# Performance work log

Measured on AMD Instinct MI355X. Metric: run time of the kernel, lower is better.

The kernel has to match this reference:

```python
import jax, jax.numpy as jnp
import numpy as np

M = 19
DIM = 768
D = DIM // 2  # r=2 -> 384
EPS = 1e-5


def _bn_eval(h, gamma, beta):
    # eval-mode BatchNorm1d with running_mean=0, running_var=1
    return h * (gamma / jnp.sqrt(1.0 + EPS)) + beta


def setup_inputs() -> dict:
    key = jax.random.key(0)
    ks = jax.random.split(key, 24)
    s = 0.02
    inp = {
        "x": jax.random.normal(ks[0], (4096, M * DIM), jnp.float32),
        "g": jax.random.normal(ks[1], (4096, M * DIM), jnp.float32),
        # fc: Linear(768,384) -> ReLU -> BN(384) -> Linear(384,384)
        "fc1_W": jax.random.normal(ks[2], (D, DIM), jnp.float32) * s,
        "fc1_b": jnp.zeros((D,), jnp.float32),
        "bn1_g": jnp.ones((D,), jnp.float32),
        "bn1_b": jnp.zeros((D,), jnp.float32),
        "fc2_W": jax.random.normal(ks[3], (D, D), jnp.float32) * s,
        "fc2_b": jnp.zeros((D,), jnp.float32),
        # 19 branch Linears fcs: (d,d); g_fcs: (dim+d, dim)
        "fcs_W": jax.random.normal(ks[4], (M, D, D), jnp.float32) * s,
        "fcs_b": jnp.zeros((M, D), jnp.float32),
        "gfcs_W": jax.random.normal(ks[5], (M, DIM, DIM + D), jnp.float32) * s,
        "gfcs_b": jnp.zeros((M, DIM), jnp.float32),
        # classifier head (numpy_class=20 < 30): 768->128->32->20
        "l1_W": jax.random.normal(ks[6], (128, DIM), jnp.float32) * s,
        "l1_b": jnp.zeros((128,), jnp.float32),
        "bna_g": jnp.ones((128,), jnp.float32),
        "bna_b": jnp.zeros((128,), jnp.float32),
        "l2_W": jax.random.normal(ks[7], (32, 128), jnp.float32) * s,
        "l2_b": jnp.zeros((32,), jnp.float32),
        "bnb_g": jnp.ones((32,), jnp.float32),
        "bnb_b": jnp.zeros((32,), jnp.float32),
        "l3_W": jax.random.normal(ks[8], (20, 32), jnp.float32) * s,
        "l3_b": jnp.zeros((20,), jnp.float32),
    }
    return inp


def reference(x, g, fc1_W, fc1_b, bn1_g, bn1_b, fc2_W, fc2_b,
              fcs_W, fcs_b, gfcs_W, gfcs_b,
              l1_W, l1_b, bna_g, bna_b, l2_W, l2_b, bnb_g, bnb_b, l3_W, l3_b):
    bs = x.shape[0]
    x3 = x.reshape(bs, M, DIM)
    g3 = g.reshape(bs, M, DIM)

    # selective_ts_with_g
    fea_u = jnp.sum(x3, axis=1)                              # (bs, 768)
    h = jax.nn.relu(fea_u @ fc1_W.T + fc1_b)
    h = _bn_eval(h, bn1_g, bn1_b)
    fea_z = h @ fc2_W.T + fc2_b                              # (bs, 384)

    # 19 branch small GEMMs, batched
    vec = jnp.einsum('bd,mod->bmo', fea_z, fcs_W) + fcs_b    # (bs, 19, 384)
    cat = jnp.concatenate([vec, g3], axis=-1)                # (bs, 19, 1152)
    att = jnp.einsum('bmi,moi->bmo', cat, gfcs_W) + gfcs_b   # (bs, 19, 768)
    att = jax.nn.softmax(att, axis=1)                        # softmax over 19 branches
    fea_v = jnp.sum(x3 * att, axis=1)                        # (bs, 768)

    # classifier head
    h = jax.nn.relu(fea_v @ l1_W.T + l1_b)
    h = _bn_eval(h, bna_g, bna_b)
    h = jax.nn.relu(h @ l2_W.T + l2_b)
    h = _bn_eval(h, bnb_g, bnb_b)
    return h @ l3_W.T + l3_b                                 # (bs, 20)
```

## Files before the change

### kernel.cpp

```cpp
#include <hip/hip_runtime.h>


typedef unsigned short u16;
typedef unsigned int u32;
typedef float f32x4 __attribute__((ext_vector_type(4)));
typedef __bf16 bf16x8 __attribute__((ext_vector_type(8)));

#define GPTR(p) ((const __attribute__((address_space(1))) void*)(p))
#define SPTR(p) ((__attribute__((address_space(3))) void*)(p))

__device__ __forceinline__ u16 f2bf(float f) {
    u32 u = __float_as_uint(f);
    u += 0x7fffu + ((u >> 16) & 1u);
    return (u16)(u >> 16);
}
__device__ __forceinline__ float bf2f(u16 h) {
    return __uint_as_float(((u32)h) << 16);
}

#define BNRS 0.9999950000374997f

#define EPI_BIAS    0
#define EPI_RELU_BN 1

template <int EPI>
__global__ __launch_bounds__(256)
void gemm_bf16_kernel(const u16* __restrict__ A, const u16* __restrict__ B,
                      const float* __restrict__ bias,
                      const float* __restrict__ bnG, const float* __restrict__ bnB,
                      u16* __restrict__ C, int K, int N)
{
    constexpr int BK = 32;
    __shared__ __align__(16) u16 lA[128 * BK];
    __shared__ __align__(16) u16 lB[128 * BK];

    const int tid  = threadIdx.x;
    const int wave = tid >> 6;
    const int lane = tid & 63;
    const int bm   = blockIdx.x * 128;
    const int bn   = blockIdx.y * 128;
    const int wm   = (wave >> 1) * 64;
    const int wn   = (wave & 1) * 64;
    const int rl   = lane & 15;
    const int qk   = (lane >> 4) * 8;

    f32x4 acc[4][4] = {};

    const u16* Ab = A + (size_t)bm * K;
    const u16* Bb = B + (size_t)bn * K;

    for (int k0 = 0; k0 < K; k0 += BK) {
#pragma unroll
        for (int r = 0; r < 2; ++r) {
            const int c   = r * 256 + wave * 64 + lane;
            const int row = c >> 2;
            const int kc  = (c & 3) << 3;
            const u16* sa = Ab + (size_t)row * K + (k0 + kc);
            const u16* sb = Bb + (size_t)row * K + (k0 + kc);
            __builtin_amdgcn_global_load_lds(GPTR(sa), SPTR(&lA[(r * 256 + wave * 64) * 8]), 16, 0, 0);
            __builtin_amdgcn_global_load_lds(GPTR(sb), SPTR(&lB[(r * 256 + wave * 64) * 8]), 16, 0, 0);
        }
        __syncthreads();

        bf16x8 af[4], bfr[4];
#pragma unroll
        for (int i = 0; i < 4; ++i) af[i]  = *(const bf16x8*)&lA[(wm + i * 16 + rl) * BK + qk];
#pragma unroll
        for (int j = 0; j < 4; ++j) bfr[j] = *(const bf16x8*)&lB[(wn + j * 16 + rl) * BK + qk];
#pragma unroll
        for (int i = 0; i < 4; ++i)
#pragma unroll
            for (int j = 0; j < 4; ++j)
                acc[i][j] = __builtin_amdgcn_mfma_f32_16x16x32_bf16(af[i], bfr[j], acc[i][j], 0, 0, 0);
        __syncthreads();
    }

    const int q4 = (lane >> 4) * 4;
#pragma unroll
    for (int j = 0; j < 4; ++j) {
        const int col = bn + wn + j * 16 + rl;
        const float bsv = bias[col];
        float scl = 1.f, sft = 0.f;
        if constexpr (EPI == EPI_RELU_BN) { scl = bnG[col] * BNRS; sft = bnB[col]; }
#pragma unroll
        for (int i = 0; i < 4; ++i) {
            const int row0 = bm + wm + i * 16 + q4;
#pragma unroll
            for (int r = 0; r < 4; ++r) {
                float v = acc[i][j][r] + bsv;
                if constexpr (EPI == EPI_RELU_BN) v = fmaxf(v, 0.f) * scl + sft;
                C[(size_t)(row0 + r) * N + col] = f2bf(v);
            }
        }
    }
}

__global__ __launch_bounds__(256)
void att_gemm_kernel(const u16* __restrict__ vec, const float* __restrict__ g,
                     const u16* __restrict__ W, const float* __restrict__ bias,
                     u16* __restrict__ att)
{
    constexpr int BK = 32, K = 1152;
    __shared__ __align__(16) u16 lA[128 * BK];
    __shared__ __align__(16) u16 lB[128 * BK];

    const int m    = blockIdx.z;
    const int tid  = threadIdx.x;
    const int wave = tid >> 6;
    const int lane = tid & 63;
    const int bm   = blockIdx.x * 128;
    const int bn   = blockIdx.y * 128;
    const int wm   = (wave >> 1) * 64;
    const int wn   = (wave & 1) * 64;
    const int rl   = lane & 15;
    const int qk   = (lane >> 4) * 8;

    f32x4 acc[4][4] = {};

    const u16*  Av = vec + (size_t)bm * 7296 + m * 384;
    const float* Ag = g  + (size_t)bm * 14592 + m * 768;
    const u16*  Bb = W  + (size_t)m * 884736 + (size_t)bn * K;

    for (int k0 = 0; k0 < K; k0 += BK) {
        if (k0 < 384) {
#pragma unroll
            for (int r = 0; r < 2; ++r) {
                const int c   = r * 256 + wave * 64 + lane;
                const int row = c >> 2;
                const int kc  = (c & 3) << 3;
                const u16* sa = Av + (size_t)row * 7296 + (k0 + kc);
                __builtin_amdgcn_global_load_lds(GPTR(sa), SPTR(&lA[(r * 256 + wave * 64) * 8]), 16, 0, 0);
            }
        } else {
#pragma unroll
            for (int r = 0; r < 2; ++r) {
                const int c   = r * 256 + tid;
                const int row = c >> 2;
                const int kc  = (c & 3) << 3;
                const float* sf = Ag + (size_t)row * 14592 + (k0 - 384 + kc);
                const float4 f0 = *(const float4*)sf;
                const float4 f1 = *(const float4*)(sf + 4);
                uint4 pk;
                pk.x = (u32)f2bf(f0.x) | ((u32)f2bf(f0.y) << 16);
                pk.y = (u32)f2bf(f0.z) | ((u32)f2bf(f0.w) << 16);
                pk.z = (u32)f2bf(f1.x) | ((u32)f2bf(f1.y) << 16);
                pk.w = (u32)f2bf(f1.z) | ((u32)f2bf(f1.w) << 16);
                *(uint4*)&lA[c * 8] = pk;
            }
        }
#pragma unroll
        for (int r = 0; r < 2; ++r) {
            const int c   = r * 256 + wave * 64 + lane;
            const int row = c >> 2;
            const int kc  = (c & 3) << 3;
            const u16* sb = Bb + (size_t)row * K + (k0 + kc);
            __builtin_amdgcn_global_load_lds(GPTR(sb), SPTR(&lB[(r * 256 + wave * 64) * 8]), 16, 0, 0);
        }
        __syncthreads();

        bf16x8 af[4], bfr[4];
#pragma unroll
        for (int i = 0; i < 4; ++i) af[i]  = *(const bf16x8*)&lA[(wm + i * 16 + rl) * BK + qk];
#pragma unroll
        for (int j = 0; j < 4; ++j) bfr[j] = *(const bf16x8*)&lB[(wn + j * 16 + rl) * BK + qk];
#pragma unroll
        for (int i = 0; i < 4; ++i)
#pragma unroll
            for (int j = 0; j < 4; ++j)
                acc[i][j] = __builtin_amdgcn_mfma_f32_16x16x32_bf16(af[i], bfr[j], acc[i][j], 0, 0, 0);
        __syncthreads();
    }

    const int q4 = (lane >> 4) * 4;
#pragma unroll
    for (int j = 0; j < 4; ++j) {
        const int col = bn + wn + j * 16 + rl;
        const float bsv = bias[(size_t)m * 768 + col];
#pragma unroll
        for (int i = 0; i < 4; ++i) {
            const int row0 = bm + wm + i * 16 + q4;
#pragma unroll
            for (int r = 0; r < 4; ++r) {
                att[(size_t)(row0 + r) * 14592 + m * 768 + col] = f2bf(acc[i][j][r] + bsv);
            }
        }
    }
}

__global__ __launch_bounds__(256)
void cvt_weights_kernel(const float* __restrict__ s0, const float* __restrict__ s1,
                        const float* __restrict__ s2, const float* __restrict__ s3,
                        const float* __restrict__ s4,
                        u16* __restrict__ d0, u16* __restrict__ d1, u16* __restrict__ d2,
                        u16* __restrict__ d3, u16* __restrict__ d4)
{
    const int i = blockIdx.x * 256 + threadIdx.x;
    const float* s; u16* d; int off;
    if (i < 294912)        { s = s0; d = d0; off = i; }
    else if (i < 442368)   { s = s1; d = d1; off = i - 294912; }
    else if (i < 3244032)  { s = s2; d = d2; off = i - 442368; }
    else if (i < 20054016) { s = s3; d = d3; off = i - 3244032; }
    else                   { s = s4; d = d4; off = i - 20054016; }
    d[off] = f2bf(s[off]);
}

__global__ __launch_bounds__(256)
void feau_kernel(const float* __restrict__ x, u16* __restrict__ feau)
{
    const int b = blockIdx.x;
    const int o = blockIdx.y * 256 + threadIdx.x;
    const float* xp = x + (size_t)b * 14592 + o;
    float s = 0.f;
#pragma unroll
    for (int m = 0; m < 19; ++m) s += xp[m * 768];
    feau[(size_t)b * 768 + o] = f2bf(s);
}

__global__ __launch_bounds__(256)
void softmax_feav_kernel(const u16* __restrict__ att, const float* __restrict__ x,
                         u16* __restrict__ feav)
{
    const int b = blockIdx.x;
    const int o = blockIdx.y * 256 + threadIdx.x;
    const u16* ap   = att + (size_t)b * 14592 + o;
    const float* xp = x   + (size_t)b * 14592 + o;
    float l[19];
    float mx = -1e30f;
#pragma unroll
    for (int m = 0; m < 19; ++m) { l[m] = bf2f(ap[m * 768]); mx = fmaxf(mx, l[m]); }
    float s = 0.f;
#pragma unroll
    for (int m = 0; m < 19; ++m) { const float e = __expf(l[m] - mx); l[m] = e; s += e; }
    const float inv = 1.f / s;
    float a = 0.f;
#pragma unroll
    for (int m = 0; m < 19; ++m) a += xp[m * 768] * l[m];
    feav[(size_t)b * 768 + o] = f2bf(a * inv);
}

__global__ __launch_bounds__(256)
void l2_kernel(const u16* __restrict__ h1, const float* __restrict__ W,
               const float* __restrict__ bias, const float* __restrict__ bg,
               const float* __restrict__ bb, float* __restrict__ h2)
{
    const int idx = blockIdx.x * 256 + threadIdx.x;
    const int b = idx >> 5, n = idx & 31;
    const u16* hp  = h1 + (size_t)b * 128;
    const float* wp = W + n * 128;
    float a = bias[n];
#pragma unroll 8
    for (int k = 0; k < 128; ++k) a += bf2f(hp[k]) * wp[k];
    a = fmaxf(a, 0.f) * (bg[n] * BNRS) + bb[n];
    h2[idx] = a;
}

__global__ __launch_bounds__(256)
void l3_kernel(const float* __restrict__ h2, const float* __restrict__ W,
               const float* __restrict__ bias, float* __restrict__ out)
{
    const int idx = blockIdx.x * 256 + threadIdx.x;
    const int b = idx / 20, n = idx - b * 20;
    const float* hp = h2 + (size_t)b * 32;
    const float* wp = W + n * 32;
    float a = bias[n];
#pragma unroll
    for (int k = 0; k < 32; ++k) a += hp[k] * wp[k];
    out[idx] = a;
}

extern "C" void kernel_launch(void* const* d_in, const int* in_sizes, int n_in,
                              void* d_out, int out_size, void* d_ws, size_t ws_size,
                              hipStream_t stream)
{
    const float* x      = (const float*)d_in[0];
    const float* g      = (const float*)d_in[1];
    const float* fc1_W  = (const float*)d_in[2];
    const float* fc1_b  = (const float*)d_in[3];
    const float* bn1_g  = (const float*)d_in[4];
    const float* bn1_b  = (const float*)d_in[5];
    const float* fc2_W  = (const float*)d_in[6];
    const float* fc2_b  = (const float*)d_in[7];
    const float* fcs_W  = (const float*)d_in[8];
    const float* fcs_b  = (const float*)d_in[9];
    const float* gfcs_W = (const float*)d_in[10];
    const float* gfcs_b = (const float*)d_in[11];
    const float* l1_W   = (const float*)d_in[12];
    const float* l1_b   = (const float*)d_in[13];
    const float* bna_g  = (const float*)d_in[14];
    const float* bna_b  = (const float*)d_in[15];
    const float* l2_W   = (const float*)d_in[16];
    const float* l2_b   = (const float*)d_in[17];
    const float* bnb_g  = (const float*)d_in[18];
    const float* bnb_b  = (const float*)d_in[19];
    const float* l3_W   = (const float*)d_in[20];
    const float* l3_b   = (const float*)d_in[21];
    float* out = (float*)d_out;

    char* w = (char*)d_ws;
    size_t off = 0;
    auto alloc = [&](size_t bytes) { void* p = w + off; off += (bytes + 255) & ~(size_t)255; return p; };
    u16* fc1w  = (u16*)alloc(294912ull * 2);
    u16* fc2w  = (u16*)alloc(147456ull * 2);
    u16* fcsw  = (u16*)alloc(2801664ull * 2);
    u16* gfcsw = (u16*)alloc(16809984ull * 2);
    u16* l1w   = (u16*)alloc(98304ull * 2);
    u16* feau  = (u16*)alloc(3145728ull * 2);
    u16* hbuf  = (u16*)alloc(1572864ull * 2);
    u16* feaz  = (u16*)alloc(1572864ull * 2);
    u16* vecb  = (u16*)alloc(29884416ull * 2);
    u16* attb  = (u16*)alloc(59768832ull * 2);
    u16* feav  = (u16*)alloc(3145728ull * 2);
    u16* h1b   = (u16*)alloc(524288ull * 2);
    float* h2f = (float*)alloc(131072ull * 4);
    (void)ws_size; (void)in_sizes; (void)n_in; (void)out_size;

    cvt_weights_kernel<<<78720, 256, 0, stream>>>(fc1_W, fc2_W, fcs_W, gfcs_W, l1_W,
                                                  fc1w, fc2w, fcsw, gfcsw, l1w);
    feau_kernel<<<dim3(4096, 3), 256, 0, stream>>>(x, feau);
    gemm_bf16_kernel<EPI_RELU_BN><<<dim3(32, 3), 256, 0, stream>>>(feau, fc1w, fc1_b, bn1_g, bn1_b, hbuf, 768, 384);
    gemm_bf16_kernel<EPI_BIAS><<<dim3(32, 3), 256, 0, stream>>>(hbuf, fc2w, fc2_b, nullptr, nullptr, feaz, 384, 384);
    gemm_bf16_kernel<EPI_BIAS><<<dim3(32, 57), 256, 0, stream>>>(feaz, fcsw, fcs_b, nullptr, nullptr, vecb, 384, 7296);
    att_gemm_kernel<<<dim3(32, 6, 19), 256, 0, stream>>>(vecb, g, gfcsw, gfcs_b, attb);
    softmax_feav_kernel<<<dim3(4096, 3), 256, 0, stream>>>(attb, x, feav);
    gemm_bf16_kernel<EPI_RELU_BN><<<dim3(32, 1), 256, 0, stream>>>(feav, l1w, l1_b, bna_g, bna_b, h1b, 768, 128);
    l2_kernel<<<512, 256, 0, stream>>>(h1b, l2_W, l2_b, bnb_g, bnb_b, h2f);
    l3_kernel<<<320, 256, 0, stream>>>(h2f, l3_W, l3_b, out);
}
```

Measured before the change: 968.6 us.

## Fold per-branch fcs weights into gfcs weights and pre-convert g to bf16

Composes each branch's fcs Linear with the first 384 columns of its gfcs weight (W1·Wfcs) once per call, with the fcs bias folded into a combined bias. This removes the vec GEMM and its large intermediate buffer, and the attention GEMM now reads fea_z directly. When workspace allows, g is converted to bf16 in a separate pass so the attention GEMM can use async global-to-LDS loads for all of K. feau and softmax are vectorised to 4 elements per thread. The weight-composition GEMM and the g conversion are extra work done on every call.

```diff
diff --git a/kernel.cpp b/kernel.cpp
--- a/kernel.cpp
+++ b/kernel.cpp
@@ -3,6 +3,7 @@
 
 typedef unsigned short u16;
 typedef unsigned int u32;
+typedef long long i64;
 typedef float f32x4 __attribute__((ext_vector_type(4)));
 typedef __bf16 bf16x8 __attribute__((ext_vector_type(8)));
 
@@ -17,23 +18,29 @@
 __device__ __forceinline__ float bf2f(u16 h) {
     return __uint_as_float(((u32)h) << 16);
 }
+__device__ __forceinline__ u32 pk2(float a, float b) {
+    return (u32)f2bf(a) | ((u32)f2bf(b) << 16);
+}
 
 #define BNRS 0.9999950000374997f
 
-#define EPI_BIAS    0
-#define EPI_RELU_BN 1
+#define EPI_NONE    0
+#define EPI_BIAS    1
+#define EPI_RELU_BN 2
 
 template <int EPI>
 __global__ __launch_bounds__(256)
-void gemm_bf16_kernel(const u16* __restrict__ A, const u16* __restrict__ B,
+void gemm_bf16_kernel(const u16* __restrict__ A, i64 Abat, int lda,
+                      const u16* __restrict__ B, i64 Bbat, int ldb,
                       const float* __restrict__ bias,
                       const float* __restrict__ bnG, const float* __restrict__ bnB,
-                      u16* __restrict__ C, int K, int N)
+                      u16* __restrict__ C, i64 Cbat, int ldc, int K)
 {
     constexpr int BK = 32;
     __shared__ __align__(16) u16 lA[128 * BK];
     __shared__ __align__(16) u16 lB[128 * BK];
 
+    const int z    = blockIdx.z;
     const int tid  = threadIdx.x;
     const int wave = tid >> 6;
     const int lane = tid & 63;
@@ -46,8 +53,8 @@
 
     f32x4 acc[4][4] = {};
 
-    const u16* Ab = A + (size_t)bm * K;
-    const u16* Bb = B + (size_t)bn * K;
+    const u16* Ab = A + (size_t)z * Abat + (size_t)bm * lda;
+    const u16* Bb = B + (size_t)z * Bbat + (size_t)bn * ldb;
 
     for (int k0 = 0; k0 < K; k0 += BK) {
 #pragma unroll
@@ -55,8 +62,8 @@
             const int c   = r * 256 + wave * 64 + lane;
             const int row = c >> 2;
             const int kc  = (c & 3) << 3;
-            const u16* sa = Ab + (size_t)row * K + (k0 + kc);
-            const u16* sb = Bb + (size_t)row * K + (k0 + kc);
+            const u16* sa = Ab + (size_t)row * lda + (k0 + kc);
+            const u16* sb = Bb + (size_t)row * ldb + (k0 + kc);
             __builtin_amdgcn_global_load_lds(GPTR(sa), SPTR(&lA[(r * 256 + wave * 64) * 8]), 16, 0, 0);
             __builtin_amdgcn_global_load_lds(GPTR(sb), SPTR(&lB[(r * 256 + wave * 64) * 8]), 16, 0, 0);
         }
@@ -75,30 +82,32 @@
         __syncthreads();
     }
 
+    u16* Cb = C + (size_t)z * Cbat;
     const int q4 = (lane >> 4) * 4;
 #pragma unroll
     for (int j = 0; j < 4; ++j) {
         const int col = bn + wn + j * 16 + rl;
-        const float bsv = bias[col];
-        float scl = 1.f, sft = 0.f;
+        float bsv = 0.f, scl = 1.f, sft = 0.f;
+        if constexpr (EPI != EPI_NONE) bsv = bias[col];
         if constexpr (EPI == EPI_RELU_BN) { scl = bnG[col] * BNRS; sft = bnB[col]; }
 #pragma unroll
         for (int i = 0; i < 4; ++i) {
             const int row0 = bm + wm + i * 16 + q4;
 #pragma unroll
             for (int r = 0; r < 4; ++r) {
-                float v = acc[i][j][r] + bsv;
+                float v = acc[i][j][r];
+                if constexpr (EPI != EPI_NONE) v += bsv;
                 if constexpr (EPI == EPI_RELU_BN) v = fmaxf(v, 0.f) * scl + sft;
-                C[(size_t)(row0 + r) * N + col] = f2bf(v);
+                Cb[(size_t)(row0 + r) * ldc + col] = f2bf(v);
             }
         }
     }
 }
 
 __global__ __launch_bounds__(256)
-void att_gemm_kernel(const u16* __restrict__ vec, const float* __restrict__ g,
-                     const u16* __restrict__ W, const float* __restrict__ bias,
-                     u16* __restrict__ att)
+void att_gemm_a_kernel(const u16* __restrict__ feaz, const u16* __restrict__ gb,
+                       const u16* __restrict__ W, const float* __restrict__ bc,
+                       u16* __restrict__ att)
 {
     constexpr int BK = 32, K = 1152;
     __shared__ __align__(16) u16 lA[128 * BK];
@@ -117,9 +126,78 @@
 
     f32x4 acc[4][4] = {};
 
-    const u16*  Av = vec + (size_t)bm * 7296 + m * 384;
-    const float* Ag = g  + (size_t)bm * 14592 + m * 768;
-    const u16*  Bb = W  + (size_t)m * 884736 + (size_t)bn * K;
+    const u16* A1 = feaz + (size_t)bm * 384;
+    const u16* A2 = gb + (size_t)bm * 14592 + m * 768;
+    const u16* Bb = W + (size_t)m * 884736 + (size_t)bn * K;
+
+    for (int k0 = 0; k0 < K; k0 += BK) {
+#pragma unroll
+        for (int r = 0; r < 2; ++r) {
+            const int c   = r * 256 + wave * 64 + lane;
+            const int row = c >> 2;
+            const int kc  = (c & 3) << 3;
+            const u16* sa = (k0 < 384)
+                ? A1 + (size_t)row * 384 + (k0 + kc)
+                : A2 + (size_t)row * 14592 + (k0 - 384 + kc);
+            const u16* sb = Bb + (size_t)row * K + (k0 + kc);
+            __builtin_amdgcn_global_load_lds(GPTR(sa), SPTR(&lA[(r * 256 + wave * 64) * 8]), 16, 0, 0);
+            __builtin_amdgcn_global_load_lds(GPTR(sb), SPTR(&lB[(r * 256 + wave * 64) * 8]), 16, 0, 0);
+        }
+        __syncthreads();
+
+        bf16x8 af[4], bfr[4];
+#pragma unroll
+        for (int i = 0; i < 4; ++i) af[i]  = *(const bf16x8*)&lA[(wm + i * 16 + rl) * BK + qk];
+#pragma unroll
+        for (int j = 0; j < 4; ++j) bfr[j] = *(const bf16x8*)&lB[(wn + j * 16 + rl) * BK + qk];
+#pragma unroll
+        for (int i = 0; i < 4; ++i)
+#pragma unroll
+            for (int j = 0; j < 4; ++j)
+                acc[i][j] = __builtin_amdgcn_mfma_f32_16x16x32_bf16(af[i], bfr[j], acc[i][j], 0, 0, 0);
+        __syncthreads();
+    }
+
+    const int q4 = (lane >> 4) * 4;
+#pragma unroll
+    for (int j = 0; j < 4; ++j) {
+        const int col = bn + wn + j * 16 + rl;
+        const float bsv = bc[m * 768 + col];
+#pragma unroll
+        for (int i = 0; i < 4; ++i) {
+            const int row0 = bm + wm + i * 16 + q4;
+#pragma unroll
+            for (int r = 0; r < 4; ++r)
+                att[(size_t)(row0 + r) * 14592 + m * 768 + col] = f2bf(acc[i][j][r] + bsv);
+        }
+    }
+}
+
+__global__ __launch_bounds__(256)
+void att_gemm_b_kernel(const u16* __restrict__ feaz, const float* __restrict__ g,
+                       const u16* __restrict__ W, const float* __restrict__ bc,
+                       u16* __restrict__ att)
+{
+    constexpr int BK = 32, K = 1152;
+    __shared__ __align__(16) u16 lA[128 * BK];
+    __shared__ __align__(16) u16 lB[128 * BK];
+
+    const int m    = blockIdx.z;
+    const int tid  = threadIdx.x;
+    const int wave = tid >> 6;
+    const int lane = tid & 63;
+    const int bm   = blockIdx.x * 128;
+    const int bn   = blockIdx.y * 128;
+    const int wm   = (wave >> 1) * 64;
+    const int wn   = (wave & 1) * 64;
+    const int rl   = lane & 15;
+    const int qk   = (lane >> 4) * 8;
+
+    f32x4 acc[4][4] = {};
+
+    const u16* A1 = feaz + (size_t)bm * 384;
+    const float* Ag = g + (size_t)bm * 14592 + m * 768;
+    const u16* Bb = W + (size_t)m * 884736 + (size_t)bn * K;
 
     for (int k0 = 0; k0 < K; k0 += BK) {
         if (k0 < 384) {
@@ -128,7 +206,7 @@
                 const int c   = r * 256 + wave * 64 + lane;
                 const int row = c >> 2;
                 const int kc  = (c & 3) << 3;
-                const u16* sa = Av + (size_t)row * 7296 + (k0 + kc);
+                const u16* sa = A1 + (size_t)row * 384 + (k0 + kc);
                 __builtin_amdgcn_global_load_lds(GPTR(sa), SPTR(&lA[(r * 256 + wave * 64) * 8]), 16, 0, 0);
             }
         } else {
@@ -141,10 +219,8 @@
                 const float4 f0 = *(const float4*)sf;
                 const float4 f1 = *(const float4*)(sf + 4);
                 uint4 pk;
-                pk.x = (u32)f2bf(f0.x) | ((u32)f2bf(f0.y) << 16);
-                pk.y = (u32)f2bf(f0.z) | ((u32)f2bf(f0.w) << 16);
-                pk.z = (u32)f2bf(f1.x) | ((u32)f2bf(f1.y) << 16);
-                pk.w = (u32)f2bf(f1.z) | ((u32)f2bf(f1.w) << 16);
+                pk.x = pk2(f0.x, f0.y);  pk.y = pk2(f0.z, f0.w);
+                pk.z = pk2(f1.x, f1.y);  pk.w = pk2(f1.z, f1.w);
                 *(uint4*)&lA[c * 8] = pk;
             }
         }
@@ -175,67 +251,147 @@
 #pragma unroll
     for (int j = 0; j < 4; ++j) {
         const int col = bn + wn + j * 16 + rl;
-        const float bsv = bias[(size_t)m * 768 + col];
+        const float bsv = bc[m * 768 + col];
 #pragma unroll
         for (int i = 0; i < 4; ++i) {
             const int row0 = bm + wm + i * 16 + q4;
 #pragma unroll
-            for (int r = 0; r < 4; ++r) {
+            for (int r = 0; r < 4; ++r)
                 att[(size_t)(row0 + r) * 14592 + m * 768 + col] = f2bf(acc[i][j][r] + bsv);
-            }
-        }
-    }
-}
-
-__global__ __launch_bounds__(256)
-void cvt_weights_kernel(const float* __restrict__ s0, const float* __restrict__ s1,
-                        const float* __restrict__ s2, const float* __restrict__ s3,
-                        const float* __restrict__ s4,
-                        u16* __restrict__ d0, u16* __restrict__ d1, u16* __restrict__ d2,
-                        u16* __restrict__ d3, u16* __restrict__ d4)
+        }
+    }
+}
+
+
+__global__ __launch_bounds__(256)
+void cvt_flat_kernel(const float* __restrict__ s0, const float* __restrict__ s1,
+                     const float* __restrict__ s2,
+                     u16* __restrict__ d0, u16* __restrict__ d1, u16* __restrict__ d2)
 {
     const int i = blockIdx.x * 256 + threadIdx.x;
     const float* s; u16* d; int off;
-    if (i < 294912)        { s = s0; d = d0; off = i; }
-    else if (i < 442368)   { s = s1; d = d1; off = i - 294912; }
-    else if (i < 3244032)  { s = s2; d = d2; off = i - 442368; }
-    else if (i < 20054016) { s = s3; d = d3; off = i - 3244032; }
-    else                   { s = s4; d = d4; off = i - 20054016; }
-    d[off] = f2bf(s[off]);
-}
-
-__global__ __launch_bounds__(256)
+    if (i < 36864)      { s = s0; d = d0; off = i; }
+    else if (i < 55296) { s = s1; d = d1; off = i - 36864; }
+    else                { s = s2; d = d2; off = i - 55296; }
+    const float4 f0 = *(const float4*)(s + off * 8);
+    const float4 f1 = *(const float4*)(s + off * 8 + 4);
+    uint4 pk; pk.x = pk2(f0.x, f0.y); pk.y = pk2(f0.z, f0.w);
+    pk.z = pk2(f1.x, f1.y); pk.w = pk2(f1.z, f1.w);
+    *(uint4*)(d + off * 8) = pk;
+}
+
+__global__ __launch_bounds__(256)
+void cvt_gfcs_kernel(const float* __restrict__ gfcs, u16* __restrict__ w1,
+                     u16* __restrict__ geff)
+{
+    const int i = blockIdx.x * 256 + threadIdx.x;
+    const int r = i / 144, c = i - r * 144;
+    const float* s = gfcs + (size_t)r * 1152 + c * 8;
+    const float4 f0 = *(const float4*)s;
+    const float4 f1 = *(const float4*)(s + 4);
+    uint4 pk; pk.x = pk2(f0.x, f0.y); pk.y = pk2(f0.z, f0.w);
+    pk.z = pk2(f1.x, f1.y); pk.w = pk2(f1.z, f1.w);
+    u16* d = (c < 48) ? (w1 + (size_t)r * 384 + c * 8)
+                      : (geff + (size_t)r * 1152 + c * 8);
+    *(uint4*)d = pk;
+}
+
+__global__ __launch_bounds__(256)
+void cvt_fcsT_kernel(const float* __restrict__ fcs, u16* __restrict__ fcswT)
+{
+    const int i = blockIdx.x * 256 + threadIdx.x;
+    const int m = i / 18432, rem = i - m * 18432;
+    const int d = rem / 48, e8 = (rem - d * 48) * 8;
+    const float* s = fcs + (size_t)m * 147456 + (size_t)e8 * 384 + d;
+    float f[8];
+#pragma unroll
+    for (int j = 0; j < 8; ++j) f[j] = s[j * 384];
+    uint4 pk; pk.x = pk2(f[0], f[1]); pk.y = pk2(f[2], f[3]);
+    pk.z = pk2(f[4], f[5]); pk.w = pk2(f[6], f[7]);
+    *(uint4*)(fcswT + (size_t)m * 147456 + (size_t)d * 384 + e8) = pk;
+}
+
+__global__ __launch_bounds__(256)
+void cvt_g_kernel(const float* __restrict__ g, u16* __restrict__ gb)
+{
+    const size_t i = ((size_t)blockIdx.x * 256 + threadIdx.x) * 8;
+    const float4 f0 = *(const float4*)(g + i);
+    const float4 f1 = *(const float4*)(g + i + 4);
+    uint4 pk; pk.x = pk2(f0.x, f0.y); pk.y = pk2(f0.z, f0.w);
+    pk.z = pk2(f1.x, f1.y); pk.w = pk2(f1.z, f1.w);
+    *(uint4*)(gb + i) = pk;
+}
+
+__global__ __launch_bounds__(256)
+void bc_kernel(const float* __restrict__ gfcs, const float* __restrict__ gfcs_b,
+               const float* __restrict__ fcs_b, float* __restrict__ bc)
+{
+    const int widx = blockIdx.x * 4 + (threadIdx.x >> 6);
+    const int lane = threadIdx.x & 63;
+    const int m = widx / 768, o = widx - m * 768;
+    const float* wr = gfcs + (size_t)m * 884736 + (size_t)o * 1152;
+    const float* fb = fcs_b + m * 384;
+    float a = 0.f;
+#pragma unroll
+    for (int t = 0; t < 6; ++t) a += wr[lane + t * 64] * fb[lane + t * 64];
+#pragma unroll
+    for (int off = 32; off > 0; off >>= 1) a += __shfl_down(a, off, 64);
+    if (lane == 0) bc[widx] = gfcs_b[widx] + a;
+}
+
+__global__ __launch_bounds__(192)
 void feau_kernel(const float* __restrict__ x, u16* __restrict__ feau)
 {
     const int b = blockIdx.x;
-    const int o = blockIdx.y * 256 + threadIdx.x;
+    const int o = threadIdx.x * 4;
     const float* xp = x + (size_t)b * 14592 + o;
-    float s = 0.f;
-#pragma unroll
-    for (int m = 0; m < 19; ++m) s += xp[m * 768];
-    feau[(size_t)b * 768 + o] = f2bf(s);
-}
-
-__global__ __launch_bounds__(256)
+    float4 s = {0.f, 0.f, 0.f, 0.f};
+#pragma unroll
+    for (int m = 0; m < 19; ++m) {
+        const float4 v = *(const float4*)(xp + m * 768);
+        s.x += v.x; s.y += v.y; s.z += v.z; s.w += v.w;
+    }
+    ushort4 r; r.x = f2bf(s.x); r.y = f2bf(s.y); r.z = f2bf(s.z); r.w = f2bf(s.w);
+    *(ushort4*)(feau + (size_t)b * 768 + o) = r;
+}
+
+__global__ __launch_bounds__(192)
 void softmax_feav_kernel(const u16* __restrict__ att, const float* __restrict__ x,
                          u16* __restrict__ feav)
 {
     const int b = blockIdx.x;
-    const int o = blockIdx.y * 256 + threadIdx.x;
+    const int o = threadIdx.x * 4;
     const u16* ap   = att + (size_t)b * 14592 + o;
     const float* xp = x   + (size_t)b * 14592 + o;
-    float l[19];
-    float mx = -1e30f;
-#pragma unroll
-    for (int m = 0; m < 19; ++m) { l[m] = bf2f(ap[m * 768]); mx = fmaxf(mx, l[m]); }
-    float s = 0.f;
-#pragma unroll
-    for (int m = 0; m < 19; ++m) { const float e = __expf(l[m] - mx); l[m] = e; s += e; }
-    const float inv = 1.f / s;
-    float a = 0.f;
-#pragma unroll
-    for (int m = 0; m < 19; ++m) a += xp[m * 768] * l[m];
-    feav[(size_t)b * 768 + o] = f2bf(a * inv);
+    float4 l[19];
+    float4 mx = {-1e30f, -1e30f, -1e30f, -1e30f};
+#pragma unroll
+    for (int m = 0; m < 19; ++m) {
+        const ushort4 u = *(const ushort4*)(ap + m * 768);
+        l[m].x = bf2f(u.x); l[m].y = bf2f(u.y); l[m].z = bf2f(u.z); l[m].w = bf2f(u.w);
+        mx.x = fmaxf(mx.x, l[m].x); mx.y = fmaxf(mx.y, l[m].y);
+        mx.z = fmaxf(mx.z, l[m].z); mx.w = fmaxf(mx.w, l[m].w);
+    }
+    float4 s = {0.f, 0.f, 0.f, 0.f};
+#pragma unroll
+    for (int m = 0; m < 19; ++m) {
+        l[m].x = __expf(l[m].x - mx.x); s.x += l[m].x;
+        l[m].y = __expf(l[m].y - mx.y); s.y += l[m].y;
+        l[m].z = __expf(l[m].z - mx.z); s.z += l[m].z;
+        l[m].w = __expf(l[m].w - mx.w); s.w += l[m].w;
+    }
+    const float4 inv = {1.f / s.x, 1.f / s.y, 1.f / s.z, 1.f / s.w};
+    float4 a = {0.f, 0.f, 0.f, 0.f};
+#pragma unroll
+    for (int m = 0; m < 19; ++m) {
+        const float4 v = *(const float4*)(xp + m * 768);
+        a.x += v.x * l[m].x; a.y += v.y * l[m].y;
+        a.z += v.z * l[m].z; a.w += v.w * l[m].w;
+    }
+    ushort4 r;
+    r.x = f2bf(a.x * inv.x); r.y = f2bf(a.y * inv.y);
+    r.z = f2bf(a.z * inv.z); r.w = f2bf(a.w * inv.w);
+    *(ushort4*)(feav + (size_t)b * 768 + o) = r;
 }
 
 __global__ __launch_bounds__(256)
@@ -295,34 +451,51 @@
     const float* l3_W   = (const float*)d_in[20];
     const float* l3_b   = (const float*)d_in[21];
     float* out = (float*)d_out;
+    (void)in_sizes; (void)n_in; (void)out_size;
 
     char* w = (char*)d_ws;
     size_t off = 0;
     auto alloc = [&](size_t bytes) { void* p = w + off; off += (bytes + 255) & ~(size_t)255; return p; };
     u16* fc1w  = (u16*)alloc(294912ull * 2);
     u16* fc2w  = (u16*)alloc(147456ull * 2);
-    u16* fcsw  = (u16*)alloc(2801664ull * 2);
-    u16* gfcsw = (u16*)alloc(16809984ull * 2);
     u16* l1w   = (u16*)alloc(98304ull * 2);
+    u16* fcswT = (u16*)alloc(2801664ull * 2);
+    u16* w1bf  = (u16*)alloc(5603328ull * 2);
+    u16* geff  = (u16*)alloc(16809984ull * 2);
+    float* bcb = (float*)alloc(14592ull * 4);
     u16* feau  = (u16*)alloc(3145728ull * 2);
     u16* hbuf  = (u16*)alloc(1572864ull * 2);
     u16* feaz  = (u16*)alloc(1572864ull * 2);
-    u16* vecb  = (u16*)alloc(29884416ull * 2);
     u16* attb  = (u16*)alloc(59768832ull * 2);
     u16* feav  = (u16*)alloc(3145728ull * 2);
     u16* h1b   = (u16*)alloc(524288ull * 2);
     float* h2f = (float*)alloc(131072ull * 4);
-    (void)ws_size; (void)in_sizes; (void)n_in; (void)out_size;
-
-    cvt_weights_kernel<<<78720, 256, 0, stream>>>(fc1_W, fc2_W, fcs_W, gfcs_W, l1_W,
-                                                  fc1w, fc2w, fcsw, gfcsw, l1w);
-    feau_kernel<<<dim3(4096, 3), 256, 0, stream>>>(x, feau);
-    gemm_bf16_kernel<EPI_RELU_BN><<<dim3(32, 3), 256, 0, stream>>>(feau, fc1w, fc1_b, bn1_g, bn1_b, hbuf, 768, 384);
-    gemm_bf16_kernel<EPI_BIAS><<<dim3(32, 3), 256, 0, stream>>>(hbuf, fc2w, fc2_b, nullptr, nullptr, feaz, 384, 384);
-    gemm_bf16_kernel<EPI_BIAS><<<dim3(32, 57), 256, 0, stream>>>(feaz, fcsw, fcs_b, nullptr, nullptr, vecb, 384, 7296);
-    att_gemm_kernel<<<dim3(32, 6, 19), 256, 0, stream>>>(vecb, g, gfcsw, gfcs_b, attb);
-    softmax_feav_kernel<<<dim3(4096, 3), 256, 0, stream>>>(attb, x, feav);
-    gemm_bf16_kernel<EPI_RELU_BN><<<dim3(32, 1), 256, 0, stream>>>(feav, l1w, l1_b, bna_g, bna_b, h1b, 768, 128);
+    u16* gbf   = (u16*)alloc(59768832ull * 2);
+    const bool useA = (ws_size >= off);
+
+    cvt_flat_kernel<<<264, 256, 0, stream>>>(fc1_W, fc2_W, l1_W, fc1w, fc2w, l1w);
+    cvt_gfcs_kernel<<<8208, 256, 0, stream>>>(gfcs_W, w1bf, geff);
+    cvt_fcsT_kernel<<<1368, 256, 0, stream>>>(fcs_W, fcswT);
+    bc_kernel<<<3648, 256, 0, stream>>>(gfcs_W, gfcs_b, fcs_b, bcb);
+    gemm_bf16_kernel<EPI_NONE><<<dim3(6, 3, 19), 256, 0, stream>>>(
+        w1bf, 294912, 384, fcswT, 147456, 384, nullptr, nullptr, nullptr,
+        geff, 884736, 1152, 384);
+    if (useA) cvt_g_kernel<<<29184, 256, 0, stream>>>(g, gbf);
+
+    feau_kernel<<<4096, 192, 0, stream>>>(x, feau);
+    gemm_bf16_kernel<EPI_RELU_BN><<<dim3(32, 3), 256, 0, stream>>>(
+        feau, 0, 768, fc1w, 0, 768, fc1_b, bn1_g, bn1_b, hbuf, 0, 384, 768);
+    gemm_bf16_kernel<EPI_BIAS><<<dim3(32, 3), 256, 0, stream>>>(
+        hbuf, 0, 384, fc2w, 0, 384, fc2_b, nullptr, nullptr, feaz, 0, 384, 384);
+
+    if (useA)
+        att_gemm_a_kernel<<<dim3(32, 6, 19), 256, 0, stream>>>(feaz, gbf, geff, bcb, attb);
+    else
+        att_gemm_b_kernel<<<dim3(32, 6, 19), 256, 0, stream>>>(feaz, g, geff, bcb, attb);
+    softmax_feav_kernel<<<4096, 192, 0, stream>>>(attb, x, feav);
+
+    gemm_bf16_kernel<EPI_RELU_BN><<<dim3(32, 1), 256, 0, stream>>>(
+        feav, 0, 768, l1w, 0, 768, l1_b, bna_g, bna_b, h1b, 0, 128, 768);
     l2_kernel<<<512, 256, 0, stream>>>(h1b, l2_W, l2_b, bnb_g, bnb_b, h2f);
     l3_kernel<<<320, 256, 0, stream>>>(h2f, l3_W, l3_b, out);
 }
```

Measured after the change: 930.6 us. 3.9% less time.
